# Kernel optimization log

Measured on AMD Instinct MI355X. Metric: run time of the kernel, lower is better.

The kernel has to match this reference:

```python
import jax, jax.numpy as jnp
import numpy as np

EPS = 1e-6
NUM_HEADS = 16

def layernorm(x, alpha, bias):
    # Faithful to the torch module: torch.std uses ddof=1, and eps is added to std.
    mean = jnp.mean(x, axis=-1, keepdims=True)
    std = jnp.std(x, axis=-1, keepdims=True, ddof=1)
    return alpha * (x - mean) / (std + EPS) + bias

def setup_inputs() -> dict:
    key = jax.random.key(0)
    B, S, D, F = 4, 2048, 1024, 4096
    ks = jax.random.split(key, 8)
    s = 1.0 / np.sqrt(D)
    inp = {
        'x': jax.random.normal(ks[0], (B, S, D), jnp.float32),
        'src_mask': jnp.ones((B, 1, 1, S), jnp.int32),
        'wq': jax.random.normal(ks[1], (D, D), jnp.float32) * s,
        'bq': jnp.zeros((D,), jnp.float32),
        'wk': jax.random.normal(ks[2], (D, D), jnp.float32) * s,
        'bk': jnp.zeros((D,), jnp.float32),
        'wv': jax.random.normal(ks[3], (D, D), jnp.float32) * s,
        'bv': jnp.zeros((D,), jnp.float32),
        'wo': jax.random.normal(ks[4], (D, D), jnp.float32) * s,
        'bo': jnp.zeros((D,), jnp.float32),
        'w1': jax.random.normal(ks[5], (D, F), jnp.float32) * s,
        'b1': jnp.zeros((F,), jnp.float32),
        'w2': jax.random.normal(ks[6], (F, D), jnp.float32) * (1.0 / np.sqrt(F)),
        'b2': jnp.zeros((D,), jnp.float32),
        'ln1_a': jnp.ones((D,), jnp.float32),
        'ln1_b': jnp.zeros((D,), jnp.float32),
        'ln2_a': jnp.ones((D,), jnp.float32),
        'ln2_b': jnp.zeros((D,), jnp.float32),
    }
    return inp

def mha(x, src_mask, wq, bq, wk, bk, wv, bv, wo, bo):
    B, S, D = x.shape
    H = NUM_HEADS
    dk = D // H
    q = (x @ wq + bq).reshape(B, S, H, dk).transpose(0, 2, 1, 3)  # [B,H,S,dk]
    k = (x @ wk + bk).reshape(B, S, H, dk).transpose(0, 2, 1, 3)
    v = (x @ wv + bv).reshape(B, S, H, dk).transpose(0, 2, 1, 3)
    scores = jnp.einsum('bhqd,bhkd->bhqk', q, k) / np.sqrt(dk)  # [B,H,S,S]
    scores = jnp.where(src_mask == 0, -1e9, scores)
    p = jax.nn.softmax(scores, axis=-1)
    ctx = jnp.einsum('bhqk,bhkd->bhqd', p, v)  # [B,H,S,dk]
    ctx = ctx.transpose(0, 2, 1, 3).reshape(B, S, D)
    return ctx @ wo + bo

def reference(x, src_mask, wq, bq, wk, bk, wv, bv, wo, bo,
              w1, b1, w2, b2, ln1_a, ln1_b, ln2_a, ln2_b):
    # residual 1: pre-norm self-attention (dropout is identity in eval)
    h = x + mha(layernorm(x, ln1_a, ln1_b), src_mask, wq, bq, wk, bk, wv, bv, wo, bo)
    # residual 2: pre-norm FFN
    hn = layernorm(h, ln2_a, ln2_b)
    ffn = jax.nn.relu(hn @ w1 + b1) @ w2 + b2
    return h + ffn
```

## Files before the change

kernel.cpp:

```cpp
#include <hip/hip_runtime.h>
#include <hip/hip_bf16.h>

typedef __attribute__((ext_vector_type(8))) short bf16x8;
typedef __attribute__((ext_vector_type(4))) short bf16x4;
typedef __attribute__((ext_vector_type(4))) float f32x4;
typedef __hip_bfloat16 bf16;
typedef unsigned short u16;

#define B_ 4
#define S_ 2048
#define D_ 1024
#define F_ 4096
#define H_ 16
#define MROWS 8192
#define QSCALE 0.18033688011116012f

__device__ __forceinline__ unsigned pkbf(float lo, float hi){
  union{float f; unsigned u;} a, b; a.f = lo; b.f = hi;
  return __builtin_amdgcn_perm(b.u + 0x8000u, a.u + 0x8000u, 0x07060302);
}
__device__ __forceinline__ u16 bfrnd(float f){
  union{float ff; unsigned u;} c; c.ff = f;
  return (u16)((c.u + 0x8000u) >> 16);
}
__device__ __forceinline__ void gll16(const bf16* gp, u16* lp){
  __builtin_amdgcn_global_load_lds(
      (const __attribute__((address_space(1))) void*)gp,
      (__attribute__((address_space(3))) void*)lp, 16, 0, 0);
}

struct PrepArgs { const float* w[6]; const float* b[3]; };
__global__ __launch_bounds__(256) void prep(
    PrepArgs pa, bf16* __restrict__ wqkvoT, bf16* __restrict__ w1T,
    bf16* __restrict__ w2T, float* __restrict__ bqkv)
{
  __shared__ float tl[32][33];
  const int bid = blockIdx.x, tid = threadIdx.x;
  const int x = tid&31, y = tid>>5;
  if (bid < 12288) {
    const float* W; bf16* dst; int K, N, nb, kb;
    if (bid < 4096)      { int wi=bid>>10, t=bid&1023; W=pa.w[wi]; dst=wqkvoT+(size_t)wi*1048576; K=1024; N=1024; nb=t&31;  kb=t>>5; }
    else if (bid < 8192) { int t=bid-4096;             W=pa.w[4];  dst=w1T;  K=1024; N=4096; nb=t&127; kb=t>>7; }
    else                 { int t=bid-8192;             W=pa.w[5];  dst=w2T;  K=4096; N=1024; nb=t&31;  kb=t>>5; }
    const int n0=nb*32, k0=kb*32;
    #pragma unroll
    for (int i=0;i<32;i+=8)
      tl[y+i][x] = W[(size_t)(k0+y+i)*N + n0+x];
    __syncthreads();
    #pragma unroll
    for (int i=0;i<32;i+=8)
      dst[(size_t)(n0+y+i)*K + k0+x] = __float2bfloat16(tl[x][y+i]);
  } else {
    for (int i=tid; i<3072; i+=256) bqkv[i] = pa.b[i>>10][i&1023];
  }
}

__global__ __launch_bounds__(256) void v_transpose(
    const bf16* __restrict__ qkv, bf16* __restrict__ vT)
{
  __shared__ u16 tile[64*65];
  const int bh = blockIdx.y, b = bh>>4, h = bh&15;
  const int s0 = blockIdx.x*64;
  const int tid = threadIdx.x;
  const bf16* src = qkv + (size_t)(b*S_ + s0)*3072 + 2048 + h*64;
  #pragma unroll
  for (int i=0;i<2;i++){
    int idx = i*256 + tid;
    int r = idx>>3, sg = idx&7;
    uint4 v = *reinterpret_cast<const uint4*>(src + (size_t)r*3072 + sg*8);
    const u16* e = (const u16*)&v;
    #pragma unroll
    for (int j=0;j<8;j++) tile[r*65 + sg*8 + j] = e[j];
  }
  __syncthreads();
  bf16* dst = vT + (size_t)bh*64*S_ + s0;
  #pragma unroll
  for (int i=0;i<2;i++){
    int idx = i*256 + tid;
    int d = idx>>3, sg = idx&7;
    u16 tmp[8];
    #pragma unroll
    for (int j=0;j<8;j++) tmp[j] = tile[(sg*8+j)*65 + d];
    *reinterpret_cast<uint4*>(dst + (size_t)d*S_ + sg*8) = *reinterpret_cast<uint4*>(tmp);
  }
}

__device__ __forceinline__ float block_reduce_256(float v, float* sbuf){
  #pragma unroll
  for (int o=32;o>0;o>>=1) v += __shfl_down(v, o);
  int wave = threadIdx.x>>6;
  if ((threadIdx.x&63)==0) sbuf[wave] = v;
  __syncthreads();
  float r = sbuf[0]+sbuf[1]+sbuf[2]+sbuf[3];
  __syncthreads();
  return r;
}

__global__ __launch_bounds__(256) void ln_fwd(
    const float* __restrict__ x, const float* __restrict__ alpha,
    const float* __restrict__ beta, bf16* __restrict__ out)
{
  __shared__ float sbuf[4];
  int row = blockIdx.x, tid = threadIdx.x;
  const float4* xr = reinterpret_cast<const float4*>(x + (size_t)row*D_);
  float4 v = xr[tid];
  float sum = block_reduce_256(v.x+v.y+v.z+v.w, sbuf);
  float mean = sum * (1.0f/1024.0f);
  float dx0=v.x-mean, dx1=v.y-mean, dx2=v.z-mean, dx3=v.w-mean;
  float ssq = block_reduce_256(dx0*dx0+dx1*dx1+dx2*dx2+dx3*dx3, sbuf);
  float std_ = sqrtf(ssq * (1.0f/1023.0f));
  float inv = 1.0f/(std_ + 1e-6f);
  const float4* ar = reinterpret_cast<const float4*>(alpha);
  const float4* br = reinterpret_cast<const float4*>(beta);
  float4 a = ar[tid], bb = br[tid];
  unsigned* o = reinterpret_cast<unsigned*>(out + (size_t)row*D_);
  o[tid*2+0] = pkbf(a.x*dx0*inv + bb.x, a.y*dx1*inv + bb.y);
  o[tid*2+1] = pkbf(a.z*dx2*inv + bb.z, a.w*dx3*inv + bb.w);
}

template<int EPI>
__global__ __launch_bounds__(512) void gemm_bt(
    const bf16* __restrict__ A, const bf16* __restrict__ BT,
    const float* __restrict__ bias, const float* __restrict__ res,
    void* __restrict__ out, int M, int N, int K)
{
  __shared__ __align__(16) u16 As[128*32];
  __shared__ __align__(16) u16 Bs[128*32];
  const int tid = threadIdx.x;
  const int m0 = blockIdx.x*128, n0 = blockIdx.y*128;
  const int wave = tid>>6, lane = tid&63;
  const int wm = (wave>>2)*64, wn = (wave&3)*32;
  const int lrow = lane&15, quad = lane>>4;
  const int srow = wave*16 + (lane>>2);
  const int sseg = lane&3;
  const bf16* apg = A  + (size_t)(m0+srow)*K + sseg*8;
  const bf16* bpg = BT + (size_t)(n0+srow)*K + sseg*8;
  u16* asd = &As[wave*512];
  u16* bsd = &Bs[wave*512];

  f32x4 acc[4][2];
  #pragma unroll
  for (int i=0;i<4;i++)
    #pragma unroll
    for (int j=0;j<2;j++) acc[i][j] = (f32x4){0.f,0.f,0.f,0.f};

  for (int k0=0; k0<K; k0+=32) {
    gll16(apg + k0, asd);
    gll16(bpg + k0, bsd);
    __syncthreads();
    bf16x8 a[4], b[2];
    #pragma unroll
    for (int t=0;t<4;t++)
      a[t] = *reinterpret_cast<const bf16x8*>(&As[(wm + t*16 + lrow)*32 + quad*8]);
    #pragma unroll
    for (int t=0;t<2;t++)
      b[t] = *reinterpret_cast<const bf16x8*>(&Bs[(wn + t*16 + lrow)*32 + quad*8]);
    #pragma unroll
    for (int mt=0;mt<4;mt++)
      #pragma unroll
      for (int nt=0;nt<2;nt++)
        acc[mt][nt] = __builtin_amdgcn_mfma_f32_16x16x32_bf16(a[mt], b[nt], acc[mt][nt], 0,0,0);
    __syncthreads();
  }

  #pragma unroll
  for (int mt=0;mt<4;mt++){
    #pragma unroll
    for (int nt=0;nt<2;nt++){
      int col = n0 + wn + nt*16 + lrow;
      float bv = bias[col];
      float sc = (EPI == 3 && col < 1024) ? QSCALE : 1.0f;
      #pragma unroll
      for (int r=0;r<4;r++){
        int row = m0 + wm + mt*16 + quad*4 + r;
        size_t idx = (size_t)row*N + col;
        float val = acc[mt][nt][r] + bv;
        if (EPI == 1) val = fmaxf(val, 0.0f);
        if (EPI == 3) val *= sc;
        if (EPI == 2) {
          ((float*)out)[idx] = val + res[idx];
        } else {
          ((u16*)out)[idx] = bfrnd(val);
        }
      }
    }
  }
}

#define LA256(bu,hf) (lds + (((bu)*2+0)*2+(hf))*8192)
#define LB256(bu,hf) (lds + (((bu)*2+1)*2+(hf))*8192)

__device__ __forceinline__ bf16x8 ldfrag(const u16* base, int row, int chunk){
  int pc = chunk ^ (row & 7);
  return *reinterpret_cast<const bf16x8*>(base + row*64 + pc*8);
}

__device__ __forceinline__ void stage_half256(const bf16* __restrict__ src, int K,
                                              u16* lbase, int wave, int lane){
  #pragma unroll
  for (int i=0;i<2;i++){
    int q = i*512 + wave*64 + lane;
    int row = q>>3;
    int seg = (q&7) ^ (row&7);
    gll16(src + (size_t)row*K + seg*8, lbase + (i*512 + wave*64)*8);
  }
}

template<int RH, int KS, bool RB, typename STG, typename TAIL>
__device__ __forceinline__ void gphase(const u16* pa, const u16* pb, int bcol,
    int lr, int quad, bf16x8 (&b)[4][2], f32x4 (&acc)[8][4], STG stg, TAIL tail)
{
  bf16x8 a_[4];
  #pragma unroll
  for (int ar=0; ar<4; ar++)
    a_[ar] = ldfrag(pa, RH*64 + ar*16 + lr, KS*4 + quad);
  if constexpr (RB){
    #pragma unroll
    for (int cb=0; cb<4; cb++){
      b[cb][0] = ldfrag(pb, bcol + cb*16 + lr, quad);
      b[cb][1] = ldfrag(pb, bcol + cb*16 + lr, 4 + quad);
    }
  }
  stg();
  __builtin_amdgcn_s_barrier();
  asm volatile("s_waitcnt lgkmcnt(0)" ::: "memory");
  __builtin_amdgcn_sched_barrier(0);
  __builtin_amdgcn_s_setprio(1);
  #pragma unroll
  for (int ar=0; ar<4; ar++)
    #pragma unroll
    for (int cb=0; cb<4; cb++)
      acc[RH*4+ar][cb] = __builtin_amdgcn_mfma_f32_16x16x32_bf16(a_[ar], b[cb][KS], acc[RH*4+ar][cb], 0,0,0);
  __builtin_amdgcn_s_setprio(0);
  tail();
  __builtin_amdgcn_s_barrier();
}

template<int EPI>
__global__ __launch_bounds__(512) void gemm256(
    const bf16* __restrict__ A, const bf16* __restrict__ BT,
    const float* __restrict__ bias, bf16* __restrict__ out, int N, int K)
{
  __shared__ __align__(16) u16 lds[65536];
  const int tid = threadIdx.x, wave = tid>>6, lane = tid&63;
  const int wr = wave>>2, wc = wave&3;
  const int lr = lane&15, quad = lane>>4;
  const int gx = gridDim.x;
  const int nwg = gx*gridDim.y;
  int flat = blockIdx.y*gx + blockIdx.x;
  int cpx = nwg>>3;
  int swz = (flat&7)*cpx + (flat>>3);
  const int m0 = (swz % gx)*256, n0 = (swz / gx)*256;
  const int T = K>>6;

  const bf16* Ag = A  + (size_t)m0*K;
  const bf16* Bg = BT + (size_t)n0*K;
  const int bcol = (wc&1)*64;

  f32x4 acc[8][4];
  #pragma unroll
  for (int i=0;i<8;i++)
    #pragma unroll
    for (int j=0;j<4;j++) acc[i][j] = (f32x4){0.f,0.f,0.f,0.f};

  stage_half256(Ag,                       K, LA256(0,0), wave, lane);
  stage_half256(Ag + (size_t)128*K,       K, LA256(0,1), wave, lane);
  stage_half256(Bg,                       K, LB256(0,0), wave, lane);
  stage_half256(Bg + (size_t)128*K,       K, LB256(0,1), wave, lane);
  stage_half256(Bg + 64,                  K, LB256(1,0), wave, lane);
  stage_half256(Bg + (size_t)128*K + 64,  K, LB256(1,1), wave, lane);
  asm volatile("s_waitcnt vmcnt(4)" ::: "memory");
  __builtin_amdgcn_s_barrier();

  for (int t=0; t<T; ++t){
    const int bu = t&1, nbu = bu^1;
    const u16* pa = LA256(bu, wr);
    const u16* pb = LB256(bu, wc>>1);
    const size_t ktA = (size_t)((t+1 < T) ? t+1 : T-1)*64;
    const size_t ktB = (size_t)((t+2 < T) ? t+2 : T-1)*64;
    bf16x8 b[4][2];
    gphase<0,0,true >(pa, pb, bcol, lr, quad, b, acc,
        [&]{ stage_half256(Ag + ktA,                 K, LA256(nbu,0), wave, lane); }, [&]{});
    gphase<1,0,false>(pa, pb, bcol, lr, quad, b, acc,
        [&]{ stage_half256(Ag + (size_t)128*K + ktA, K, LA256(nbu,1), wave, lane); }, [&]{});
    gphase<0,1,false>(pa, pb, bcol, lr, quad, b, acc,
        [&]{ stage_half256(Bg + ktB,                 K, LB256(bu,0),  wave, lane); }, [&]{});
    gphase<1,1,false>(pa, pb, bcol, lr, quad, b, acc,
        [&]{ stage_half256(Bg + (size_t)128*K + ktB, K, LB256(bu,1),  wave, lane); },
        [&]{ asm volatile("s_waitcnt vmcnt(4)" ::: "memory"); });
  }

  #pragma unroll
  for (int mi=0; mi<8; mi++){
    const int row0 = m0 + wr*128 + (mi>>2)*64 + (mi&3)*16 + quad*4;
    #pragma unroll
    for (int cb=0; cb<4; cb++){
      const int col = n0 + wc*64 + cb*16 + lr;
      float bv = bias[col];
      float sc = (EPI==3 && col < 1024) ? QSCALE : 1.0f;
      #pragma unroll
      for (int r=0; r<4; r++){
        float val = acc[mi][cb][r] + bv;
        if (EPI == 1) val = fmaxf(val, 0.0f);
        if (EPI == 3) val *= sc;
        ((u16*)out)[(size_t)(row0+r)*N + col] = bfrnd(val);
      }
    }
  }
}

#define LA2(bu,hf) (lds2 + ((bu)*3+(hf))*8192)
#define LB2(bu)    (lds2 + ((bu)*3+2)*8192)

template<int RH, int KS, bool RB, typename STG, typename TAIL>
__device__ __forceinline__ void gphase2(const u16* pa, const u16* pb, int bcol,
    int lr, int quad, bf16x8 (&b)[2][2], f32x4 (&acc)[8][2], STG stg, TAIL tail)
{
  bf16x8 a_[4];
  #pragma unroll
  for (int ar=0; ar<4; ar++)
    a_[ar] = ldfrag(pa, RH*64 + ar*16 + lr, KS*4 + quad);
  if constexpr (RB){
    #pragma unroll
    for (int cb=0; cb<2; cb++){
      b[cb][0] = ldfrag(pb, bcol + cb*16 + lr, quad);
      b[cb][1] = ldfrag(pb, bcol + cb*16 + lr, 4 + quad);
    }
  }
  stg();
  __builtin_amdgcn_s_barrier();
  asm volatile("s_waitcnt lgkmcnt(0)" ::: "memory");
  __builtin_amdgcn_sched_barrier(0);
  __builtin_amdgcn_s_setprio(1);
  #pragma unroll
  for (int ar=0; ar<4; ar++)
    #pragma unroll
    for (int cb=0; cb<2; cb++)
      acc[RH*4+ar][cb] = __builtin_amdgcn_mfma_f32_16x16x32_bf16(a_[ar], b[cb][KS], acc[RH*4+ar][cb], 0,0,0);
  __builtin_amdgcn_s_setprio(0);
  tail();
  __builtin_amdgcn_s_barrier();
}

__global__ __launch_bounds__(512) void gemm256r(
    const bf16* __restrict__ A, const bf16* __restrict__ BT,
    const float* __restrict__ bias, const float* __restrict__ res,
    float* __restrict__ out, int N, int K)
{
  __shared__ __align__(16) u16 lds2[49152];
  const int tid = threadIdx.x, wave = tid>>6, lane = tid&63;
  const int wr = wave>>2, wc = wave&3;
  const int lr = lane&15, quad = lane>>4;
  const int gx = gridDim.x;
  const int nwg = gx*gridDim.y;
  int flat = blockIdx.y*gx + blockIdx.x;
  int cpx = nwg>>3;
  int swz = (flat&7)*cpx + (flat>>3);
  const int m0 = (swz % gx)*256, n0 = (swz / gx)*128;
  const int T = K>>6;

  const bf16* Ag = A  + (size_t)m0*K;
  const bf16* Bg = BT + (size_t)n0*K;
  const int bcol = wc*32;

  f32x4 acc[8][2];
  #pragma unroll
  for (int i=0;i<8;i++)
    #pragma unroll
    for (int j=0;j<2;j++) acc[i][j] = (f32x4){0.f,0.f,0.f,0.f};

  stage_half256(Ag,                 K, LA2(0,0), wave, lane);
  stage_half256(Ag + (size_t)128*K, K, LA2(0,1), wave, lane);
  stage_half256(Bg,                 K, LB2(0),   wave, lane);
  stage_half256(Bg + 64,            K, LB2(1),   wave, lane);
  asm volatile("s_waitcnt vmcnt(2)" ::: "memory");
  __builtin_amdgcn_s_barrier();

  for (int t=0; t<T; ++t){
    const int bu = t&1, nbu = bu^1;
    const u16* pa = LA2(bu, wr);
    const u16* pb = LB2(bu);
    const size_t ktA = (size_t)((t+1 < T) ? t+1 : T-1)*64;
    const size_t ktB = (size_t)((t+2 < T) ? t+2 : T-1)*64;
    bf16x8 b[2][2];
    gphase2<0,0,true >(pa, pb, bcol, lr, quad, b, acc,
        [&]{ stage_half256(Ag + ktA,                 K, LA2(nbu,0), wave, lane); }, [&]{});
    gphase2<1,0,false>(pa, pb, bcol, lr, quad, b, acc,
        [&]{ stage_half256(Ag + (size_t)128*K + ktA, K, LA2(nbu,1), wave, lane); }, [&]{});
    gphase2<0,1,false>(pa, pb, bcol, lr, quad, b, acc,
        [&]{ stage_half256(Bg + ktB,                 K, LB2(bu),    wave, lane); }, [&]{});
    gphase2<1,1,false>(pa, pb, bcol, lr, quad, b, acc,
        [&]{}, [&]{ asm volatile("s_waitcnt vmcnt(2)" ::: "memory"); });
  }

  #pragma unroll
  for (int mi=0; mi<8; mi++){
    const int row0 = m0 + wr*128 + (mi>>2)*64 + (mi&3)*16 + quad*4;
    #pragma unroll
    for (int cb=0; cb<2; cb++){
      const int col = n0 + bcol + cb*16 + lr;
      float bv = bias[col];
      #pragma unroll
      for (int r=0; r<4; r++){
        size_t idx = (size_t)(row0+r)*N + col;
        out[idx] = acc[mi][cb][r] + bv + res[idx];
      }
    }
  }
}

#define KP 72

__global__ __launch_bounds__(512) void flash_attn_mfma(
    const bf16* __restrict__ qkv, const bf16* __restrict__ vT,
    const int* __restrict__ mask, bf16* __restrict__ ctx)
{
  __shared__ __align__(16) u16 Ks[2][64*KP];
  __shared__ __align__(16) u16 Vt[2][64*KP];
  __shared__ __align__(16) float Mb[2][64];

  const int b = blockIdx.z, h = blockIdx.y, qt = blockIdx.x;
  const int tid = threadIdx.x, wave = tid>>6, lane = tid&63;
  const int lr = lane&15, quad = lane>>4;
  const int qbase = qt*256 + wave*32;

  const bf16* base = qkv + (size_t)b*S_*3072 + h*64;
  const bf16* vtb  = vT + (size_t)(b*H_+h)*64*S_;
  const int*  mrow = mask + b*S_;

  bf16x8 qf[2][2];
  #pragma unroll
  for (int c=0;c<2;c++){
    const bf16* qp = base + (size_t)(qbase + c*16 + lr)*3072 + quad*8;
    qf[c][0] = *reinterpret_cast<const bf16x8*>(qp);
    qf[c][1] = *reinterpret_cast<const bf16x8*>(qp + 32);
  }

  const bf16x4 ones4 = {(short)0x3F80,(short)0x3F80,(short)0x3F80,(short)0x3F80};

  f32x4 actx[2][4];
  f32x4 acc_l[2];
  #pragma unroll
  for (int c=0;c<2;c++){
    #pragma unroll
    for (int dt=0;dt<4;dt++) actx[c][dt] = (f32x4){0.f,0.f,0.f,0.f};
    acc_l[c] = (f32x4){0.f,0.f,0.f,0.f};
  }

  const int sr = tid>>3, sg = tid&7;
  const bf16* kgp = base + 1024 + (size_t)sr*3072 + sg*8;
  const bf16* vgp = vtb + (size_t)sr*S_ + sg*8;

  {
    uint4 k0 = *reinterpret_cast<const uint4*>(kgp);
    uint4 v0 = *reinterpret_cast<const uint4*>(vgp);
    *reinterpret_cast<uint4*>(&Ks[0][sr*KP + sg*8]) = k0;
    *reinterpret_cast<uint4*>(&Vt[0][sr*KP + sg*8]) = v0;
  }
  int mcur = mrow[lane];
  if (tid < 64) Mb[0][tid] = (mcur==0) ? -2e9f : 0.0f;
  __syncthreads();

  int ti = 0;
  for (int kt=0; kt<S_; kt+=64, ti^=1){
    const bool more = (kt+64 < S_);
    uint4 kreg, vreg; int mnext = 1;
    if (more){
      kreg = *reinterpret_cast<const uint4*>(kgp + (size_t)(kt+64)*3072);
      vreg = *reinterpret_cast<const uint4*>(vgp + kt + 64);
      mnext = mrow[kt + 64 + lane];
    }
    unsigned long long bal = __ballot(mcur == 0);

    bf16x4 pk[2][4];
    if (bal == 0ULL) {
      #pragma unroll
      for (int nt=0;nt<4;nt++){
        bf16x8 kf0 = *reinterpret_cast<const bf16x8*>(&Ks[ti][(nt*16+lr)*KP + quad*8]);
        bf16x8 kf1 = *reinterpret_cast<const bf16x8*>(&Ks[ti][(nt*16+lr)*KP + 32 + quad*8]);
        #pragma unroll
        for (int c=0;c<2;c++){
          f32x4 a = (f32x4){0.f,0.f,0.f,0.f};
          a = __builtin_amdgcn_mfma_f32_16x16x32_bf16(kf0, qf[c][0], a, 0,0,0);
          a = __builtin_amdgcn_mfma_f32_16x16x32_bf16(kf1, qf[c][1], a, 0,0,0);
          uint2 w;
          w.x = pkbf(__builtin_amdgcn_exp2f(a[0]), __builtin_amdgcn_exp2f(a[1]));
          w.y = pkbf(__builtin_amdgcn_exp2f(a[2]), __builtin_amdgcn_exp2f(a[3]));
          union{uint2 u; bf16x4 v;} cvt; cvt.u = w;
          pk[c][nt] = cvt.v;
        }
      }
    } else {
      #pragma unroll
      for (int nt=0;nt<4;nt++){
        bf16x8 kf0 = *reinterpret_cast<const bf16x8*>(&Ks[ti][(nt*16+lr)*KP + quad*8]);
        bf16x8 kf1 = *reinterpret_cast<const bf16x8*>(&Ks[ti][(nt*16+lr)*KP + 32 + quad*8]);
        float4 mb = *reinterpret_cast<const float4*>(&Mb[ti][nt*16 + quad*4]);
        #pragma unroll
        for (int c=0;c<2;c++){
          f32x4 a = (f32x4){0.f,0.f,0.f,0.f};
          a = __builtin_amdgcn_mfma_f32_16x16x32_bf16(kf0, qf[c][0], a, 0,0,0);
          a = __builtin_amdgcn_mfma_f32_16x16x32_bf16(kf1, qf[c][1], a, 0,0,0);
          uint2 w;
          w.x = pkbf(__builtin_amdgcn_exp2f(a[0]+mb.x), __builtin_amdgcn_exp2f(a[1]+mb.y));
          w.y = pkbf(__builtin_amdgcn_exp2f(a[2]+mb.z), __builtin_amdgcn_exp2f(a[3]+mb.w));
          union{uint2 u; bf16x4 v;} cvt; cvt.u = w;
          pk[c][nt] = cvt.v;
        }
      }
    }

    #pragma unroll
    for (int dt=0;dt<4;dt++){
      #pragma unroll
      for (int kc=0;kc<4;kc++){
        bf16x4 vf = *reinterpret_cast<const bf16x4*>(&Vt[ti][(dt*16+lr)*KP + kc*16 + quad*4]);
        #pragma unroll
        for (int c=0;c<2;c++)
          actx[c][dt] = __builtin_amdgcn_mfma_f32_16x16x16bf16_1k(vf, pk[c][kc], actx[c][dt], 0,0,0);
      }
    }
    #pragma unroll
    for (int kc=0;kc<4;kc++)
      #pragma unroll
      for (int c=0;c<2;c++)
        acc_l[c] = __builtin_amdgcn_mfma_f32_16x16x16bf16_1k(ones4, pk[c][kc], acc_l[c], 0,0,0);

    if (more){
      *reinterpret_cast<uint4*>(&Ks[ti^1][sr*KP + sg*8]) = kreg;
      *reinterpret_cast<uint4*>(&Vt[ti^1][sr*KP + sg*8]) = vreg;
      if (tid < 64) Mb[ti^1][tid] = (mnext==0) ? -2e9f : 0.0f;
    }
    mcur = mnext;
    __syncthreads();
  }

  #pragma unroll
  for (int c=0;c<2;c++){
    float inv = 1.0f/acc_l[c][0];
    int q = qbase + c*16 + lr;
    bf16* op = ctx + (size_t)(b*S_+q)*D_ + h*64 + quad*4;
    #pragma unroll
    for (int dt=0;dt<4;dt++){
      uint2 o;
      o.x = pkbf(actx[c][dt][0]*inv, actx[c][dt][1]*inv);
      o.y = pkbf(actx[c][dt][2]*inv, actx[c][dt][3]*inv);
      *reinterpret_cast<uint2*>(op + dt*16) = o;
    }
  }
}

extern "C" void kernel_launch(void* const* d_in, const int* in_sizes, int n_in,
                              void* d_out, int out_size, void* d_ws, size_t ws_size,
                              hipStream_t stream) {
  const float* x    = (const float*)d_in[0];
  const int*   mask = (const int*)  d_in[1];
  const float* wq   = (const float*)d_in[2];
  const float* bq   = (const float*)d_in[3];
  const float* wk   = (const float*)d_in[4];
  const float* bk   = (const float*)d_in[5];
  const float* wv   = (const float*)d_in[6];
  const float* bv   = (const float*)d_in[7];
  const float* wo   = (const float*)d_in[8];
  const float* bo   = (const float*)d_in[9];
  const float* w1   = (const float*)d_in[10];
  const float* b1   = (const float*)d_in[11];
  const float* w2   = (const float*)d_in[12];
  const float* b2   = (const float*)d_in[13];
  const float* ln1a = (const float*)d_in[14];
  const float* ln1b = (const float*)d_in[15];
  const float* ln2a = (const float*)d_in[16];
  const float* ln2b = (const float*)d_in[17];

  char* ws = (char*)d_ws;
  bf16*  wqkvT = (bf16*) (ws + 0);
  bf16*  woT   = (bf16*) (ws + 6291456);
  bf16*  w1T   = (bf16*) (ws + 8388608);
  bf16*  w2T   = (bf16*) (ws + 16777216);
  float* bqkv  = (float*)(ws + 25165824);
  bf16*  xn    = (bf16*) (ws + 25178112);
  bf16*  vT    = (bf16*) (ws + 25178112);
  bf16*  qkv   = (bf16*) (ws + 41955328);
  bf16*  ctx   = (bf16*) (ws + 92286976);
  bf16*  hn    = (bf16*) (ws + 109064192);
  bf16*  act   = (bf16*) (ws + 25178112);

  PrepArgs pa;
  pa.w[0]=wq; pa.w[1]=wk; pa.w[2]=wv; pa.w[3]=wo; pa.w[4]=w1; pa.w[5]=w2;
  pa.b[0]=bq; pa.b[1]=bk; pa.b[2]=bv;
  prep<<<12289,256,0,stream>>>(pa, wqkvT, w1T, w2T, bqkv);

  ln_fwd<<<8192,256,0,stream>>>(x, ln1a, ln1b, xn);
  gemm256<3><<<dim3(32,12),512,0,stream>>>(xn, wqkvT, bqkv, qkv, 3072, 1024);
  v_transpose<<<dim3(32,64),256,0,stream>>>(qkv, vT);
  flash_attn_mfma<<<dim3(S_/256,H_,B_),512,0,stream>>>(qkv, vT, mask, ctx);
  gemm256r<<<dim3(32,8),512,0,stream>>>(ctx, woT, bo, x, (float*)d_out, 1024, 1024);
  ln_fwd<<<8192,256,0,stream>>>((const float*)d_out, ln2a, ln2b, hn);
  gemm256<1><<<dim3(32,16),512,0,stream>>>(hn, w1T, b1, act, F_, 1024);
  gemm256r<<<dim3(32,8),512,0,stream>>>(act, w2T, b2, (const float*)d_out, (float*)d_out, 1024, 4096);
}
```

Measured before the change: 524.7 us.

## Split-K the FFN down-projection GEMM with atomic accumulation into output

Adds a gemm256s kernel that splits the K=4096 reduction of the second FFN GEMM into two halves across a grid z dimension, using 256x256 tiles. Each workgroup accumulates its partial product with fp32 atomicAdd into the output, which already holds the residual h. Only the first K-slice adds the bias. This aims to raise reuse per tile while keeping enough workgroups to fill the GPU, at the cost of atomic read-modify-write traffic and non-deterministic summation order.

Result: slower. 556.8 us (+6.1%).

```diff
diff --git a/kernel.cpp b/kernel.cpp
--- a/kernel.cpp
+++ b/kernel.cpp
@@ -304,6 +304,77 @@
         if (EPI == 1) val = fmaxf(val, 0.0f);
         if (EPI == 3) val *= sc;
         ((u16*)out)[(size_t)(row0+r)*N + col] = bfrnd(val);
+      }
+    }
+  }
+}
+
+__global__ __launch_bounds__(512) void gemm256s(
+    const bf16* __restrict__ A, const bf16* __restrict__ BT,
+    const float* __restrict__ bias, float* __restrict__ out, int N, int K, int KT)
+{
+  __shared__ __align__(16) u16 lds[65536];
+  const int tid = threadIdx.x, wave = tid>>6, lane = tid&63;
+  const int wr = wave>>2, wc = wave&3;
+  const int lr = lane&15, quad = lane>>4;
+  const int gx = gridDim.x;
+  const int nwg = gx*gridDim.y*gridDim.z;
+  int flat = (blockIdx.z*gridDim.y + blockIdx.y)*gx + blockIdx.x;
+  int cpx = nwg>>3;
+  int swz = (flat&7)*cpx + (flat>>3);
+  const int mn = gx*gridDim.y;
+  const int kz = swz / mn;
+  const int rem = swz % mn;
+  const int m0 = (rem % gx)*256, n0 = (rem / gx)*256;
+  const int T = KT>>6;
+
+  const bf16* Ag = A  + (size_t)m0*K + (size_t)kz*KT;
+  const bf16* Bg = BT + (size_t)n0*K + (size_t)kz*KT;
+  const int bcol = (wc&1)*64;
+
+  f32x4 acc[8][4];
+  #pragma unroll
+  for (int i=0;i<8;i++)
+    #pragma unroll
+    for (int j=0;j<4;j++) acc[i][j] = (f32x4){0.f,0.f,0.f,0.f};
+
+  stage_half256(Ag,                       K, LA256(0,0), wave, lane);
+  stage_half256(Ag + (size_t)128*K,       K, LA256(0,1), wave, lane);
+  stage_half256(Bg,                       K, LB256(0,0), wave, lane);
+  stage_half256(Bg + (size_t)128*K,       K, LB256(0,1), wave, lane);
+  stage_half256(Bg + 64,                  K, LB256(1,0), wave, lane);
+  stage_half256(Bg + (size_t)128*K + 64,  K, LB256(1,1), wave, lane);
+  asm volatile("s_waitcnt vmcnt(4)" ::: "memory");
+  __builtin_amdgcn_s_barrier();
+
+  for (int t=0; t<T; ++t){
+    const int bu = t&1, nbu = bu^1;
+    const u16* pa = LA256(bu, wr);
+    const u16* pb = LB256(bu, wc>>1);
+    const size_t ktA = (size_t)((t+1 < T) ? t+1 : T-1)*64;
+    const size_t ktB = (size_t)((t+2 < T) ? t+2 : T-1)*64;
+    bf16x8 b[4][2];
+    gphase<0,0,true >(pa, pb, bcol, lr, quad, b, acc,
+        [&]{ stage_half256(Ag + ktA,                 K, LA256(nbu,0), wave, lane); }, [&]{});
+    gphase<1,0,false>(pa, pb, bcol, lr, quad, b, acc,
+        [&]{ stage_half256(Ag + (size_t)128*K + ktA, K, LA256(nbu,1), wave, lane); }, [&]{});
+    gphase<0,1,false>(pa, pb, bcol, lr, quad, b, acc,
+        [&]{ stage_half256(Bg + ktB,                 K, LB256(bu,0),  wave, lane); }, [&]{});
+    gphase<1,1,false>(pa, pb, bcol, lr, quad, b, acc,
+        [&]{ stage_half256(Bg + (size_t)128*K + ktB, K, LB256(bu,1),  wave, lane); },
+        [&]{ asm volatile("s_waitcnt vmcnt(4)" ::: "memory"); });
+  }
+
+  #pragma unroll
+  for (int mi=0; mi<8; mi++){
+    const int row0 = m0 + wr*128 + (mi>>2)*64 + (mi&3)*16 + quad*4;
+    #pragma unroll
+    for (int cb=0; cb<4; cb++){
+      const int col = n0 + wc*64 + cb*16 + lr;
+      float bv = (kz==0) ? bias[col] : 0.0f;
+      #pragma unroll
+      for (int r=0; r<4; r++){
+        atomicAdd(&out[(size_t)(row0+r)*N + col], acc[mi][cb][r] + bv);
       }
     }
   }
@@ -597,5 +668,5 @@
   gemm256r<<<dim3(32,8),512,0,stream>>>(ctx, woT, bo, x, (float*)d_out, 1024, 1024);
   ln_fwd<<<8192,256,0,stream>>>((const float*)d_out, ln2a, ln2b, hn);
   gemm256<1><<<dim3(32,16),512,0,stream>>>(hn, w1T, b1, act, F_, 1024);
-  gemm256r<<<dim3(32,8),512,0,stream>>>(act, w2T, b2, (const float*)d_out, (float*)d_out, 1024, 4096);
-}
+  gemm256s<<<dim3(32,4,2),512,0,stream>>>(act, w2T, b2, (float*)d_out, 1024, 4096, 2048);
+}
```
